# Optimization experiments

Measured on AMD Instinct MI355X. Metric: run time of the kernel, lower is better.

Reference implementation:

```python
import jax, jax.numpy as jnp
from jax import lax
import numpy as np

BIG_I = jnp.int32(2 ** 30)   # background / +inf sentinel for labels
BIG_F = 1e6                  # +inf sentinel for distances (max true dist ~ H+W)


def cc_labels(fg):
    """8-connected component labeling via iterative min-label propagation.
    fg: (H, W) bool. Returns int32 labels; background pixels get BIG_I.
    Two pixels are in the same component iff their labels are equal
    (labels are min linear index of the component, which is all the loss uses)."""
    H, W = fg.shape
    lab0 = jnp.where(fg, jnp.arange(H * W, dtype=jnp.int32).reshape(H, W), BIG_I)

    def neigh_min(lab):
        p = jnp.pad(lab, 1, constant_values=BIG_I)
        m = lab
        for di in (-1, 0, 1):
            for dj in (-1, 0, 1):
                m = jnp.minimum(m, lax.dynamic_slice(p, (1 + di, 1 + dj), (H, W)))
        return jnp.where(fg, m, BIG_I)

    def body(state):
        lab, _ = state
        new = neigh_min(lab)
        return new, jnp.all(new == lab)

    lab, _ = lax.while_loop(lambda s: ~s[1], body, (lab0, jnp.array(False)))
    return lab


def _dt_axis(d, axis):
    # exact 1D L1 (min-plus, slope 1) lower envelope via forward/backward scans
    d = jnp.moveaxis(d, axis, 0)
    init = jnp.full(d.shape[1:], BIG_F, dtype=d.dtype)
    step = lambda c, x: ((jnp.minimum(x, c + 1.0),) * 2)
    _, fwd = lax.scan(step, init, d)
    _, bwd = lax.scan(step, init, d[::-1])
    return jnp.moveaxis(jnp.minimum(fwd, bwd[::-1]), 0, axis)


def l1_distance_transform(zero_mask):
    """Exact L1 distance to the nearest True pixel of zero_mask
    (== cv2.distanceTransform(DIST_L1, maskSize=3) on a binary image whose
    zero set is zero_mask). L1 DT is separable -> two 1D passes."""
    d0 = jnp.where(zero_mask, 0.0, BIG_F).astype(jnp.float32)
    return _dt_axis(_dt_axis(d0, 0), 1)


def _loss_one(result, pts):
    WEIGHT, GAP_W, CLUST_W = 100.0, 10.0, 90.0
    r0 = result[pts[0, 0], pts[0, 1]]
    r1 = result[pts[1, 0], pts[1, 1]]
    soa_inv = jnp.sum(1.0 - result)  # soa_cells_inv (per-pixel loop in original)
    fallback = (2.0 - (r0 + r1)) * WEIGHT
    loss_start = fallback

    img = lax.stop_gradient(jnp.round(result))  # result.round().detach()
    fg = img > 0.5
    lab = cc_labels(fg)
    sl = lab[pts[0, 0], pts[0, 1]]
    el = lab[pts[1, 0], pts[1, 1]]
    both = fg[pts[0, 0], pts[0, 1]] & fg[pts[1, 0], pts[1, 1]]  # start/end labels != 0

    # start_cluster = pixels of the start component (same set when start==end)
    start_mask = fg & (lab == sl) & both
    # modified label image: end component -> 0, everything else nonzero
    end_zero = fg & (lab == el)
    dist = l1_distance_transform(end_zero)  # distance to end component
    min_d = jnp.minimum(dist[pts[0, 0], pts[0, 1]],
                        jnp.min(jnp.where(start_mask, dist, BIG_F)))

    gap_loss = jnp.where(both, min_d * soa_inv * GAP_W * soa_inv, fallback)
    cluster_cells = jnp.sum(jnp.where(start_mask, result, 0.0))
    cluster_pen = jnp.where(both, cluster_cells * CLUST_W, fallback)
    return loss_start, gap_loss, cluster_pen


def setup_inputs():
    key = jax.random.key(0)
    k1, k2 = jax.random.split(key)
    result_given = jax.random.uniform(k1, (4, 1, 512, 512), dtype=jnp.float32)
    points_given = jax.random.randint(k2, (4, 2, 2), 0, 512, dtype=jnp.int32)
    return {"result_given": result_given, "points_given": points_given}


def reference(result_given, points_given):
    # Original loop overwrites loss/gap_loss/cluster_size_penalty each batch
    # iteration -> returned tuple reflects only the last batch element.
    ls, gl, cp = jax.vmap(_loss_one)(result_given[:, 0], points_given)
    return ls[-1], gl[-1], cp[-1]
```

## Files before the change

kernel.cpp:

```cpp
#include <hip/hip_runtime.h>

#define H 512
#define W 512
#define NPIX (H * W)
#define BIG_I 1073741824
#define BIG_F 1.0e6f
#define INF30 1.0e30f

struct Scal {
  float soa;
  unsigned int min_bits;
  float cluster;
  unsigned int done;
  int both;
  float r0, r1;
  int sl, p0;
  int skip;
};

__device__ __forceinline__ int rep(int* lab, int v) {
  int cur = lab[v];
  if (cur == v) return v;
  int prev = v, next;
  while (cur > (next = lab[cur])) { lab[prev] = next; prev = cur; cur = next; }
  return cur;
}
__device__ __forceinline__ void unite(int* lab, int a, int b) {
  int ra = rep(lab, a), rb = rep(lab, b);
  while (ra != rb) {
    if (ra < rb) { int t = ra; ra = rb; rb = t; }
    int old = atomicCAS(&lab[ra], ra, rb);
    if (old == ra) break;
    ra = rep(lab, old);
    rb = rep(lab, rb);
  }
}
__device__ __forceinline__ int root_ph(int* lab, int v) {
  int p = lab[v];
  if (p == v) return v;
  int gp = lab[p];
  while (p != gp) {
    lab[v] = gp;
    v = p; p = gp; gp = lab[p];
  }
  return p;
}
__device__ __forceinline__ int runstart(unsigned m, int c) {
  unsigned z = ~m & ((1u << c) - 1u);
  return z ? (32 - __clz((int)z)) : 0;
}

__global__ void k_pre(const float* __restrict__ img, const int* __restrict__ pts,
                      Scal* __restrict__ s, float* __restrict__ out) {
  if (threadIdx.x != 0) return;
  int p0 = pts[0] * W + pts[1];
  int p1 = pts[2] * W + pts[3];
  float r0 = img[p0], r1 = img[p1];
  int both = (rintf(r0) > 0.5f) && (rintf(r1) > 0.5f);
  s->both = both;
  s->r0 = r0;
  s->r1 = r1;
  s->p0 = p0;
  s->min_bits = __float_as_uint(BIG_F);
  s->cluster = 0.0f;
  s->done = 0u;
  s->skip = 0;
  if (!both) {
    float fb = (2.0f - (r0 + r1)) * 100.0f;
    out[0] = fb; out[1] = fb; out[2] = fb;
  }
}

__global__ __launch_bounds__(256) void k_local(const float* __restrict__ img,
                                               int* __restrict__ lab,
                                               float* __restrict__ Asoa,
                                               const Scal* __restrict__ s) {
  if (!s->both) return;
  __shared__ int sl[1024];
  __shared__ unsigned rmask[32];
  __shared__ float red[4];
  const int t = threadIdx.x, b = blockIdx.x;
  const int tileX = (b & 15) * 32;
  const int tileY = (b >> 4) * 32;
  const int r = t >> 3, c0 = (t & 7) * 4;
  const float4 x4 = *(const float4*)(img + (tileY + r) * W + tileX + c0);
  float acc = 4.0f - (x4.x + x4.y + x4.z + x4.w);
  unsigned nib = (rintf(x4.x) > 0.5f ? 1u : 0u) | (rintf(x4.y) > 0.5f ? 2u : 0u)
               | (rintf(x4.z) > 0.5f ? 4u : 0u) | (rintf(x4.w) > 0.5f ? 8u : 0u);
  unsigned m = nib << c0;
  m |= __shfl_xor(m, 1, 64);
  m |= __shfl_xor(m, 2, 64);
  m |= __shfl_xor(m, 4, 64);
  if ((t & 7) == 0) rmask[r] = m;
  unsigned startM = m & ~(m << 1);
  #pragma unroll
  for (int k = 0; k < 4; ++k) {
    int c = c0 + k;
    if ((startM >> c) & 1u) sl[(r << 5) + c] = (r << 5) + c;
  }
  __syncthreads();
  if (r > 0) {
    unsigned ma = rmask[r - 1];
    unsigned upM = m & ma & (~(m << 1) | ~(ma << 1));
    unsigned dL  = startM & (ma << 1) & ~ma;
    unsigned dR  = (m & ~(m >> 1)) & (ma >> 1) & ~ma;
    #pragma unroll
    for (int k = 0; k < 4; ++k) {
      int c = c0 + k;
      int myS = (r << 5) + runstart(m, c);
      if ((upM >> c) & 1u) unite(sl, myS, ((r - 1) << 5) + runstart(ma, c));
      if ((dL  >> c) & 1u) unite(sl, myS, ((r - 1) << 5) + runstart(ma, c - 1));
      if ((dR  >> c) & 1u) unite(sl, myS, ((r - 1) << 5) + c + 1);
    }
  }
  __syncthreads();
  int o[4];
  #pragma unroll
  for (int k = 0; k < 4; ++k) {
    int c = c0 + k;
    if ((m >> c) & 1u) {
      int rt = rep(sl, (r << 5) + runstart(m, c));
      o[k] = (tileY + (rt >> 5)) * W + tileX + (rt & 31);
    } else o[k] = BIG_I;
  }
  *(int4*)(lab + (tileY + r) * W + tileX + c0) = make_int4(o[0], o[1], o[2], o[3]);
  for (int off = 32; off; off >>= 1) acc += __shfl_down(acc, off, 64);
  if ((t & 63) == 0) red[t >> 6] = acc;
  __syncthreads();
  if (t == 0) Asoa[b] = red[0] + red[1] + red[2] + red[3];
}

__global__ void k_border(int* __restrict__ lab, const float* __restrict__ Asoa,
                         Scal* __restrict__ s) {
  if (!s->both) return;
  int t = threadIdx.x;
  int lane = t & 63;
  int gid = blockIdx.x * 256 + t;
  if (gid < 7680) {
    int bb = gid >> 9, j = gid & 511;
    int i = (bb + 1) * 32;
    int p = i * W + j, q = p - W;
    int a  = lab[p];
    int u0 = lab[q];
    int um = (j > 0)   ? lab[q - 1] : BIG_I;
    int up = (j < 511) ? lab[q + 1] : BIG_I;
    int a_prev = __shfl_up(a, 1, 64);
    if (lane == 0) a_prev = (j > 0) ? lab[p - 1] : BIG_I;
    if (a != BIG_I) {
      if (um != BIG_I && a != a_prev) unite(lab, a, um);
      if (u0 != BIG_I && u0 != um) unite(lab, a, u0);
      if (up != BIG_I && up != u0 && !(u0 == BIG_I && up == um)) unite(lab, a, up);
    }
  } else if (gid < 15360) {
    int t2 = gid - 7680;
    int bb = t2 >> 9, i = t2 & 511;
    int j = (bb + 1) * 32;
    int p = i * W + j;
    int lp = lab[p], ll = lab[p - 1];
    int lpp = __shfl_up(lp, 1, 64);
    int llp = __shfl_up(ll, 1, 64);
    if (lane == 0) {
      lpp = (i > 0) ? lab[p - W] : BIG_I;
      llp = (i > 0) ? lab[p - W - 1] : BIG_I;
    }
    bool fgp = lp != BIG_I, fgl = ll != BIG_I;
    if (fgp && fgl && !(lp == lpp && ll == llp)) unite(lab, lp, ll);
    if ((i & 31) && i > 0) {
      if (fgp && llp != BIG_I && lp != lpp) unite(lab, lp, llp);
      if (fgl && lpp != BIG_I && ll != llp) unite(lab, ll, lpp);
    }
  } else if (t < 64) {
    float a = Asoa[t] + Asoa[t + 64] + Asoa[t + 128] + Asoa[t + 192];
    for (int off = 32; off; off >>= 1) a += __shfl_down(a, off, 64);
    if (t == 0) s->soa = a;
  }
}

__global__ __launch_bounds__(128) void k_dt_rows(int* __restrict__ lab,
                                                 int* __restrict__ lab2,
                                                 const float* __restrict__ img,
                                                 const int* __restrict__ pts,
                                                 Scal* __restrict__ s,
                                                 float* __restrict__ dist) {
  if (!s->both) return;
  int lane = threadIdx.x & 63;
  int row = blockIdx.x * 2 + (threadIdx.x >> 6);
  int el = -1, sl2 = -1;
  if (lane == 0) {
    int p0 = pts[0] * W + pts[1], p1 = pts[2] * W + pts[3];
    el = root_ph(lab, lab[p1]);
    sl2 = root_ph(lab, lab[p0]);
    if (blockIdx.x == 0 && threadIdx.x == 0) {
      s->sl = sl2;
      s->skip = (el == sl2);
    }
  }
  el = __shfl(el, 0, 64);
  sl2 = __shfl(sl2, 0, 64);
  const bool skip = (el == sl2);
  const int4* lp = (const int4*)(lab + row * W) + lane * 2;
  int4 a = lp[0], bq = lp[1];
  int v[8] = {a.x, a.y, a.z, a.w, bq.x, bq.y, bq.z, bq.w};
  int psrc = -1, proot = -1;
  #pragma unroll
  for (int k = 0; k < 8; ++k) {
    if (v[k] == BIG_I) continue;
    if (v[k] == psrc) { v[k] = proot; continue; }
    psrc = v[k];
    proot = root_ph(lab, v[k]);
    v[k] = proot;
  }
  if (!skip) {
    int4* l2 = (int4*)(lab2 + row * W) + lane * 2;
    l2[0] = make_int4(v[0], v[1], v[2], v[3]);
    l2[1] = make_int4(v[4], v[5], v[6], v[7]);
  }
  const float4* ip = (const float4*)(img + row * W) + lane * 2;
  float4 i0q = ip[0], i1q = ip[1];
  float cv = 0.0f;
  if (v[0] == sl2) cv += i0q.x;
  if (v[1] == sl2) cv += i0q.y;
  if (v[2] == sl2) cv += i0q.z;
  if (v[3] == sl2) cv += i0q.w;
  if (v[4] == sl2) cv += i1q.x;
  if (v[5] == sl2) cv += i1q.y;
  if (v[6] == sl2) cv += i1q.z;
  if (v[7] == sl2) cv += i1q.w;
  for (int off = 32; off; off >>= 1) cv += __shfl_down(cv, off, 64);
  if (lane == 0 && cv != 0.0f) atomicAdd(&s->cluster, cv);
  if (skip) return;
  float d[8];
  #pragma unroll
  for (int k = 0; k < 8; ++k) d[k] = (v[k] == el) ? 0.0f : BIG_F;
  int j0 = lane * 8;
  float pf[8], sb[8];
  float m = INF30;
  #pragma unroll
  for (int k = 0; k < 8; ++k) { m = fminf(m, d[k] - (float)(j0 + k)); pf[k] = m; }
  float tf = m;
  m = INF30;
  #pragma unroll
  for (int k = 7; k >= 0; --k) { m = fminf(m, d[k] + (float)(j0 + k)); sb[k] = m; }
  float tb = m;
  float vv = tf;
  #pragma unroll
  for (int off = 1; off < 64; off <<= 1) {
    float u = __shfl_up(vv, off, 64);
    if (lane >= off) vv = fminf(vv, u);
  }
  float ef = __shfl_up(vv, 1, 64); if (lane == 0) ef = INF30;
  vv = tb;
  #pragma unroll
  for (int off = 1; off < 64; off <<= 1) {
    float u = __shfl_down(vv, off, 64);
    if (lane < 64 - off) vv = fminf(vv, u);
  }
  float eb = __shfl_down(vv, 1, 64); if (lane == 63) eb = INF30;
  float o[8];
  #pragma unroll
  for (int k = 0; k < 8; ++k) {
    float j = (float)(j0 + k);
    o[k] = fminf(j + fminf(ef, pf[k]), -j + fminf(eb, sb[k]));
  }
  float4* dp = (float4*)(dist + row * W) + lane * 2;
  dp[0] = make_float4(o[0], o[1], o[2], o[3]);
  dp[1] = make_float4(o[4], o[5], o[6], o[7]);
}

__global__ __launch_bounds__(512) void k_dt_colfin(
    const float* __restrict__ dist, const int* __restrict__ lab2,
    Scal* __restrict__ s, float* __restrict__ out) {
  if (!s->both) return;
  if (s->skip) {
    if (threadIdx.x == 0) {
      unsigned old = atomicAdd(&s->done, 1u);
      if (old == gridDim.x - 1) {
        out[0] = (2.0f - (s->r0 + s->r1)) * 100.0f;
        out[1] = 0.0f;
        float cl = atomicAdd(&s->cluster, 0.0f);
        out[2] = cl * 90.0f;
      }
    }
    return;
  }
  __shared__ float laf[32][16], lbb[32][16];
  __shared__ float smin[8];
  int t = threadIdx.x;
  int sg = t >> 4, c = t & 15;
  int j = blockIdx.x * 16 + c;
  int i0 = sg * 16;
  float rr[16];
  float fa = INF30, fb = INF30;
  #pragma unroll
  for (int il = 0; il < 16; ++il) {
    rr[il] = dist[(i0 + il) * W + j];
    float fi = (float)(i0 + il);
    fa = fminf(fa, rr[il] - fi);
    fb = fminf(fb, rr[il] + fi);
  }
  laf[sg][c] = fa;
  lbb[sg][c] = fb;
  __syncthreads();
  float cf = INF30, cb = INF30;
  #pragma unroll
  for (int bb = 0; bb < 32; ++bb) {
    if (bb < sg) cf = fminf(cf, laf[bb][c]);
    if (bb > sg) cb = fminf(cb, lbb[bb][c]);
  }
  int slv = s->sl;
  int p0 = s->p0;
  float ff[16];
  float m = cf;
  #pragma unroll
  for (int il = 0; il < 16; ++il) {
    float fi = (float)(i0 + il);
    m = fminf(m, rr[il] - fi);
    ff[il] = fi + m;
  }
  m = cb;
  float dv = BIG_F;
  #pragma unroll
  for (int il = 15; il >= 0; --il) {
    int pix = (i0 + il) * W + j;
    float fi = (float)(i0 + il);
    m = fminf(m, rr[il] + fi);
    float o = fminf(ff[il], m - fi);
    if (lab2[pix] == slv) dv = fminf(dv, o);
    if (pix == p0) dv = fminf(dv, o);
  }
  for (int off = 32; off; off >>= 1)
    dv = fminf(dv, __shfl_down(dv, off, 64));
  if ((t & 63) == 0) smin[t >> 6] = dv;
  __syncthreads();
  if (t == 0) {
    float mm = INF30;
    #pragma unroll
    for (int w = 0; w < 8; ++w) mm = fminf(mm, smin[w]);
    atomicMin(&s->min_bits, __float_as_uint(mm));
    __threadfence();
    unsigned old = atomicAdd(&s->done, 1u);
    if (old == gridDim.x - 1) {
      float fallback = (2.0f - (s->r0 + s->r1)) * 100.0f;
      out[0] = fallback;
      float min_d = __uint_as_float(atomicOr(&s->min_bits, 0u));
      float cl = atomicAdd(&s->cluster, 0.0f);
      float soa = s->soa;
      out[1] = min_d * soa * 10.0f * soa;
      out[2] = cl * 90.0f;
    }
  }
}

extern "C" void kernel_launch(void* const* d_in, const int* in_sizes, int n_in,
                              void* d_out, int out_size, void* d_ws, size_t ws_size,
                              hipStream_t stream) {
  const float* img = (const float*)d_in[0] + 3 * NPIX;
  const int* pts = (const int*)d_in[1] + 3 * 4;
  float* out = (float*)d_out;

  int* lab = (int*)d_ws;
  float* dist = (float*)d_ws + NPIX;
  char* base = (char*)d_ws + (size_t)2 * NPIX * 4;
  Scal* s = (Scal*)base;
  float* Asoa = (float*)(base + 64);
  int* lab2 = (int*)(base + 64 + 1024);

  k_pre<<<1, 64, 0, stream>>>(img, pts, s, out);
  k_local<<<256, 256, 0, stream>>>(img, lab, Asoa, s);
  k_border<<<61, 256, 0, stream>>>(lab, Asoa, s);
  k_dt_rows<<<H / 2, 128, 0, stream>>>(lab, lab2, img, pts, s, dist);
  k_dt_colfin<<<32, 512, 0, stream>>>(dist, lab2, s, out);
}
```

Baseline: 60.66 us.

## Fuse five-kernel pipeline into one cooperative kernel with grid syncs

Replaces the five separate launches (pre, local CCL, border merge, row DT, column DT/finalize) with a single cooperative kernel that uses grid.sync between phases. If the cooperative launch fails, it falls back to the original launches. The goal is to remove per-launch overhead and inter-kernel gaps. The cost is the price of grid-wide barriers, plus forcing all 256 blocks to be co-resident.

Result: slower. 77.69 us (+28.1%).

```diff
diff --git a/kernel.cpp b/kernel.cpp
--- a/kernel.cpp
+++ b/kernel.cpp
@@ -1,4 +1,7 @@
 #include <hip/hip_runtime.h>
+#include <hip/hip_cooperative_groups.h>
+
+namespace cg = cooperative_groups;
 
 #define H 512
 #define W 512
@@ -12,6 +15,7 @@
   unsigned int min_bits;
   float cluster;
   unsigned int done;
+  unsigned int done2;
   int both;
   float r0, r1;
   int sl, p0;
@@ -48,6 +52,297 @@
 __device__ __forceinline__ int runstart(unsigned m, int c) {
   unsigned z = ~m & ((1u << c) - 1u);
   return z ? (32 - __clz((int)z)) : 0;
+}
+
+__global__ __launch_bounds__(256) void k_mega(
+    const float* __restrict__ img, const int* __restrict__ pts,
+    int* __restrict__ lab, int* __restrict__ lab2, float* __restrict__ dist,
+    Scal* __restrict__ s, float* __restrict__ Asoa, float* __restrict__ out) {
+  cg::grid_group grid = cg::this_grid();
+  __shared__ union {
+    struct { int uf[1024]; unsigned rmask[32]; float red[4]; } p1;
+    struct { float laf[32][8]; float lbb[32][8]; float smin[4]; } p4;
+  } sh;
+  __shared__ int sflag;
+
+  const int t = threadIdx.x;
+  const int b = blockIdx.x;
+
+  const int tileX = (b & 15) * 32;
+  const int tileY = (b >> 4) * 32;
+  const int r = t >> 3, c0 = (t & 7) * 4;
+  const float4 x4 = *(const float4*)(img + (tileY + r) * W + tileX + c0);
+
+  const int p0 = pts[0] * W + pts[1];
+  const int p1x = pts[2] * W + pts[3];
+  const float r0 = img[p0], r1 = img[p1x];
+  const bool both = (rintf(r0) > 0.5f) && (rintf(r1) > 0.5f);
+  const float fb = (2.0f - (r0 + r1)) * 100.0f;
+  if (!both) {
+    if (b == 0 && t == 0) { out[0] = fb; out[1] = fb; out[2] = fb; }
+    return;
+  }
+  if (b == 0 && t == 0) {
+    s->min_bits = __float_as_uint(BIG_F);
+    s->cluster = 0.0f;
+    s->done = 0u;
+    s->done2 = 0u;
+  }
+
+  {
+    float acc = 4.0f - (x4.x + x4.y + x4.z + x4.w);
+    unsigned nib = (rintf(x4.x) > 0.5f ? 1u : 0u) | (rintf(x4.y) > 0.5f ? 2u : 0u)
+                 | (rintf(x4.z) > 0.5f ? 4u : 0u) | (rintf(x4.w) > 0.5f ? 8u : 0u);
+    unsigned m = nib << c0;
+    m |= __shfl_xor(m, 1, 64);
+    m |= __shfl_xor(m, 2, 64);
+    m |= __shfl_xor(m, 4, 64);
+    if ((t & 7) == 0) sh.p1.rmask[r] = m;
+    unsigned startM = m & ~(m << 1);
+    #pragma unroll
+    for (int k = 0; k < 4; ++k) {
+      int c = c0 + k;
+      if ((startM >> c) & 1u) sh.p1.uf[(r << 5) + c] = (r << 5) + c;
+    }
+    __syncthreads();
+    if (r > 0) {
+      unsigned ma = sh.p1.rmask[r - 1];
+      unsigned upM = m & ma & (~(m << 1) | ~(ma << 1));
+      unsigned dL  = startM & (ma << 1) & ~ma;
+      unsigned dR  = (m & ~(m >> 1)) & (ma >> 1) & ~ma;
+      #pragma unroll
+      for (int k = 0; k < 4; ++k) {
+        int c = c0 + k;
+        int myS = (r << 5) + runstart(m, c);
+        if ((upM >> c) & 1u) unite(sh.p1.uf, myS, ((r - 1) << 5) + runstart(ma, c));
+        if ((dL  >> c) & 1u) unite(sh.p1.uf, myS, ((r - 1) << 5) + runstart(ma, c - 1));
+        if ((dR  >> c) & 1u) unite(sh.p1.uf, myS, ((r - 1) << 5) + c + 1);
+      }
+    }
+    __syncthreads();
+    int o[4];
+    #pragma unroll
+    for (int k = 0; k < 4; ++k) {
+      int c = c0 + k;
+      if ((m >> c) & 1u) {
+        int rt = rep(sh.p1.uf, (r << 5) + runstart(m, c));
+        o[k] = (tileY + (rt >> 5)) * W + tileX + (rt & 31);
+      } else o[k] = BIG_I;
+    }
+    *(int4*)(lab + (tileY + r) * W + tileX + c0) = make_int4(o[0], o[1], o[2], o[3]);
+    for (int off = 32; off; off >>= 1) acc += __shfl_down(acc, off, 64);
+    if ((t & 63) == 0) sh.p1.red[t >> 6] = acc;
+    __syncthreads();
+    if (t == 0) Asoa[b] = sh.p1.red[0] + sh.p1.red[1] + sh.p1.red[2] + sh.p1.red[3];
+  }
+  grid.sync();
+
+  {
+    int lane = t & 63;
+    int gid = b * 256 + t;
+    if (gid < 7680) {
+      int bb = gid >> 9, j = gid & 511;
+      int i = (bb + 1) * 32;
+      int p = i * W + j, q = p - W;
+      int a  = lab[p];
+      int u0 = lab[q];
+      int um = (j > 0)   ? lab[q - 1] : BIG_I;
+      int up = (j < 511) ? lab[q + 1] : BIG_I;
+      int a_prev = __shfl_up(a, 1, 64);
+      if (lane == 0) a_prev = (j > 0) ? lab[p - 1] : BIG_I;
+      if (a != BIG_I) {
+        if (um != BIG_I && a != a_prev) unite(lab, a, um);
+        if (u0 != BIG_I && u0 != um) unite(lab, a, u0);
+        if (up != BIG_I && up != u0 && !(u0 == BIG_I && up == um)) unite(lab, a, up);
+      }
+    } else if (gid < 15360) {
+      int t2 = gid - 7680;
+      int bb = t2 >> 9, i = t2 & 511;
+      int j = (bb + 1) * 32;
+      int p = i * W + j;
+      int lp = lab[p], ll = lab[p - 1];
+      int lpp = __shfl_up(lp, 1, 64);
+      int llp = __shfl_up(ll, 1, 64);
+      if (lane == 0) {
+        lpp = (i > 0) ? lab[p - W] : BIG_I;
+        llp = (i > 0) ? lab[p - W - 1] : BIG_I;
+      }
+      bool fgp = lp != BIG_I, fgl = ll != BIG_I;
+      if (fgp && fgl && !(lp == lpp && ll == llp)) unite(lab, lp, ll);
+      if ((i & 31) && i > 0) {
+        if (fgp && llp != BIG_I && lp != lpp) unite(lab, lp, llp);
+        if (fgl && lpp != BIG_I && ll != llp) unite(lab, ll, lpp);
+      }
+    } else if (b == 60 && t < 64) {
+      float a = Asoa[t] + Asoa[t + 64] + Asoa[t + 128] + Asoa[t + 192];
+      for (int off = 32; off; off >>= 1) a += __shfl_down(a, off, 64);
+      if (t == 0) s->soa = a;
+    }
+  }
+  grid.sync();
+
+  if (t < 128) {
+    int lane = t & 63;
+    int row = b * 2 + (t >> 6);
+    int el = -1, sl2 = -1;
+    if (lane == 0) {
+      el = root_ph(lab, lab[p1x]);
+      sl2 = root_ph(lab, lab[p0]);
+      if (t == 0) sflag = (el == sl2);
+      if (b == 0 && t == 0) s->sl = sl2;
+    }
+    el = __shfl(el, 0, 64);
+    sl2 = __shfl(sl2, 0, 64);
+    const bool skip = (el == sl2);
+    const int4* lp = (const int4*)(lab + row * W) + lane * 2;
+    int4 a = lp[0], bq = lp[1];
+    int v[8] = {a.x, a.y, a.z, a.w, bq.x, bq.y, bq.z, bq.w};
+    int psrc = -1, proot = -1;
+    #pragma unroll
+    for (int k = 0; k < 8; ++k) {
+      if (v[k] == BIG_I) continue;
+      if (v[k] == psrc) { v[k] = proot; continue; }
+      psrc = v[k];
+      proot = root_ph(lab, v[k]);
+      v[k] = proot;
+    }
+    if (!skip) {
+      int4* l2 = (int4*)(lab2 + row * W) + lane * 2;
+      l2[0] = make_int4(v[0], v[1], v[2], v[3]);
+      l2[1] = make_int4(v[4], v[5], v[6], v[7]);
+    }
+    const float4* ip = (const float4*)(img + row * W) + lane * 2;
+    float4 i0q = ip[0], i1q = ip[1];
+    float cv = 0.0f;
+    if (v[0] == sl2) cv += i0q.x;
+    if (v[1] == sl2) cv += i0q.y;
+    if (v[2] == sl2) cv += i0q.z;
+    if (v[3] == sl2) cv += i0q.w;
+    if (v[4] == sl2) cv += i1q.x;
+    if (v[5] == sl2) cv += i1q.y;
+    if (v[6] == sl2) cv += i1q.z;
+    if (v[7] == sl2) cv += i1q.w;
+    for (int off = 32; off; off >>= 1) cv += __shfl_down(cv, off, 64);
+    if (lane == 0 && cv != 0.0f) atomicAdd(&s->cluster, cv);
+    if (!skip) {
+      float d[8];
+      #pragma unroll
+      for (int k = 0; k < 8; ++k) d[k] = (v[k] == el) ? 0.0f : BIG_F;
+      int j0 = lane * 8;
+      float pf[8], sb[8];
+      float m = INF30;
+      #pragma unroll
+      for (int k = 0; k < 8; ++k) { m = fminf(m, d[k] - (float)(j0 + k)); pf[k] = m; }
+      float tf = m;
+      m = INF30;
+      #pragma unroll
+      for (int k = 7; k >= 0; --k) { m = fminf(m, d[k] + (float)(j0 + k)); sb[k] = m; }
+      float tb = m;
+      float vv = tf;
+      #pragma unroll
+      for (int off = 1; off < 64; off <<= 1) {
+        float u = __shfl_up(vv, off, 64);
+        if (lane >= off) vv = fminf(vv, u);
+      }
+      float ef = __shfl_up(vv, 1, 64); if (lane == 0) ef = INF30;
+      vv = tb;
+      #pragma unroll
+      for (int off = 1; off < 64; off <<= 1) {
+        float u = __shfl_down(vv, off, 64);
+        if (lane < 64 - off) vv = fminf(vv, u);
+      }
+      float eb = __shfl_down(vv, 1, 64); if (lane == 63) eb = INF30;
+      float o[8];
+      #pragma unroll
+      for (int k = 0; k < 8; ++k) {
+        float j = (float)(j0 + k);
+        o[k] = fminf(j + fminf(ef, pf[k]), -j + fminf(eb, sb[k]));
+      }
+      float4* dp = (float4*)(dist + row * W) + lane * 2;
+      dp[0] = make_float4(o[0], o[1], o[2], o[3]);
+      dp[1] = make_float4(o[4], o[5], o[6], o[7]);
+    }
+  }
+  __syncthreads();
+  const bool skipb = sflag != 0;
+
+  if (skipb) {
+    if (t == 0) {
+      __threadfence();
+      unsigned old = atomicAdd(&s->done, 1u);
+      if (old == gridDim.x - 1) {
+        out[0] = fb;
+        out[1] = 0.0f;
+        float cl = atomicAdd(&s->cluster, 0.0f);
+        out[2] = cl * 90.0f;
+      }
+    }
+    return;
+  }
+  grid.sync();
+
+  if (b < 64) {
+    int sg = t >> 3, c = t & 7;
+    int j = b * 8 + c;
+    int i0 = sg * 16;
+    float rr[16];
+    float fa = INF30, fbk = INF30;
+    #pragma unroll
+    for (int il = 0; il < 16; ++il) {
+      rr[il] = dist[(i0 + il) * W + j];
+      float fi = (float)(i0 + il);
+      fa = fminf(fa, rr[il] - fi);
+      fbk = fminf(fbk, rr[il] + fi);
+    }
+    sh.p4.laf[sg][c] = fa;
+    sh.p4.lbb[sg][c] = fbk;
+    __syncthreads();
+    float cf = INF30, cb = INF30;
+    #pragma unroll
+    for (int bb = 0; bb < 32; ++bb) {
+      if (bb < sg) cf = fminf(cf, sh.p4.laf[bb][c]);
+      if (bb > sg) cb = fminf(cb, sh.p4.lbb[bb][c]);
+    }
+    int slv = s->sl;
+    float ff[16];
+    float m = cf;
+    #pragma unroll
+    for (int il = 0; il < 16; ++il) {
+      float fi = (float)(i0 + il);
+      m = fminf(m, rr[il] - fi);
+      ff[il] = fi + m;
+    }
+    m = cb;
+    float dv = BIG_F;
+    #pragma unroll
+    for (int il = 15; il >= 0; --il) {
+      int pix = (i0 + il) * W + j;
+      float fi = (float)(i0 + il);
+      m = fminf(m, rr[il] + fi);
+      float o = fminf(ff[il], m - fi);
+      if (lab2[pix] == slv) dv = fminf(dv, o);
+      if (pix == p0) dv = fminf(dv, o);
+    }
+    for (int off = 32; off; off >>= 1)
+      dv = fminf(dv, __shfl_down(dv, off, 64));
+    if ((t & 63) == 0) sh.p4.smin[t >> 6] = dv;
+    __syncthreads();
+    if (t == 0) {
+      float mm = fminf(fminf(sh.p4.smin[0], sh.p4.smin[1]),
+                       fminf(sh.p4.smin[2], sh.p4.smin[3]));
+      atomicMin(&s->min_bits, __float_as_uint(mm));
+      __threadfence();
+      unsigned old = atomicAdd(&s->done2, 1u);
+      if (old == 63u) {
+        out[0] = fb;
+        float min_d = __uint_as_float(atomicOr(&s->min_bits, 0u));
+        float cl = atomicAdd(&s->cluster, 0.0f);
+        float soa = s->soa;
+        out[1] = min_d * soa * 10.0f * soa;
+        out[2] = cl * 90.0f;
+      }
+    }
+  }
 }
 
 __global__ void k_pre(const float* __restrict__ img, const int* __restrict__ pts,
@@ -365,9 +660,16 @@
   float* Asoa = (float*)(base + 64);
   int* lab2 = (int*)(base + 64 + 1024);
 
-  k_pre<<<1, 64, 0, stream>>>(img, pts, s, out);
-  k_local<<<256, 256, 0, stream>>>(img, lab, Asoa, s);
-  k_border<<<61, 256, 0, stream>>>(lab, Asoa, s);
-  k_dt_rows<<<H / 2, 128, 0, stream>>>(lab, lab2, img, pts, s, dist);
-  k_dt_colfin<<<32, 512, 0, stream>>>(dist, lab2, s, out);
-}
+  void* ka[8] = {(void*)&img, (void*)&pts, (void*)&lab, (void*)&lab2,
+                 (void*)&dist, (void*)&s, (void*)&Asoa, (void*)&out};
+  hipError_t err = hipLaunchCooperativeKernel((const void*)k_mega, dim3(256),
+                                              dim3(256), ka, 0, stream);
+  if (err != hipSuccess) {
+    (void)hipGetLastError();
+    k_pre<<<1, 64, 0, stream>>>(img, pts, s, out);
+    k_local<<<256, 256, 0, stream>>>(img, lab, Asoa, s);
+    k_border<<<61, 256, 0, stream>>>(lab, Asoa, s);
+    k_dt_rows<<<H / 2, 128, 0, stream>>>(lab, lab2, img, pts, s, dist);
+    k_dt_colfin<<<32, 512, 0, stream>>>(dist, lab2, s, out);
+  }
+}
```
